# Kernel tuning notes

Measured on AMD Instinct MI355X. Metric: run time of the kernel, lower is better.

The kernel has to match this reference:

```python
import jax, jax.numpy as jnp
import numpy as np

EPS = 1e-5
HEADS, DK, DV, STRIDE, R = 8, 32, 32, 2, 4


def _conv(x, w, b, stride, pad, groups):
    y = jax.lax.conv_general_dilated(
        x, w, (stride, stride), [(pad, pad), (pad, pad)],
        dimension_numbers=('NCHW', 'OIHW', 'NCHW'),
        feature_group_count=groups)
    return y + b[None, :, None, None]


def _ln_chw(x):
    # torch F.layer_norm(x, [c, h, w]) with no affine: normalize over C,H,W per sample
    m = jnp.mean(x, axis=(1, 2, 3), keepdims=True)
    v = jnp.var(x, axis=(1, 2, 3), keepdims=True)
    return (x - m) * jax.lax.rsqrt(v + EPS)


def _bn(x, g, b, m, v):
    # eval-mode BatchNorm2d with running stats
    inv = jax.lax.rsqrt(v + EPS)
    return (x - m[None, :, None, None]) * (g * inv)[None, :, None, None] + b[None, :, None, None]


def _gelu(x):
    return jax.nn.gelu(x, approximate=False)  # torch nn.GELU default = exact erf


def _forward(x, lpu_w, lpu_b, dw_w, dw_b, wq, bq, wk, bk, wv, bv, wo, bo, pos_b,
             c1_w, c1_b, bn1_g, bn1_b, bn1_m, bn1_v,
             dw2_w, dw2_b, bn2_g, bn2_b, bn2_m, bn2_v,
             c2_w, c2_b, bn3_g, bn3_b, bn3_m, bn3_v):
    c = x.shape[1]
    # ---- LPU: depthwise 3x3 + residual ----
    x = _conv(x, lpu_w, lpu_b, 1, 1, c) + x
    b_, c, h, w = x.shape
    n = h * w
    # ---- LMHSA ----
    xn = _ln_chw(x)
    xr = xn.reshape(b_, c, n).transpose(0, 2, 1)                 # [b, N, c]
    q = (xr @ wq.T + bq).reshape(b_, n, HEADS, DK).transpose(0, 2, 1, 3)  # [b,H,N,dk]
    kv = _conv(x, dw_w, dw_b, STRIDE, 0, c)                      # note: on x (pre-LN), as in source
    nk = kv.shape[2] * kv.shape[3]
    kvr = kv.reshape(b_, c, nk).transpose(0, 2, 1)               # [b, Nk, c]
    k = (kvr @ wk.T + bk).reshape(b_, nk, HEADS, DK).transpose(0, 2, 1, 3)
    v = (kvr @ wv.T + bv).reshape(b_, nk, HEADS, DV).transpose(0, 2, 1, 3)
    att = jnp.einsum('bhid,bhjd->bhij', q, k) * (DK ** -0.5) + pos_b
    att = jax.nn.softmax(att, axis=-1)
    tmp = jnp.einsum('bhij,bhjd->bhid', att, v).transpose(0, 2, 1, 3).reshape(b_, n, HEADS * DV)
    # source does .view(b, d, h, w) on a contiguous [b, N, d] tensor -> raw row-major reinterpret
    x = (tmp @ wo.T + bo).reshape(b_, c, h, w) + x
    # ---- IRFFN ----
    t = _ln_chw(x)
    t = _gelu(_bn(_conv(t, c1_w, c1_b, 1, 0, 1), bn1_g, bn1_b, bn1_m, bn1_v))
    t = _gelu(_bn(_conv(t, dw2_w, dw2_b, 1, 1, t.shape[1]), bn2_g, bn2_b, bn2_m, bn2_v))
    t = _bn(_conv(t, c2_w, c2_b, 1, 0, 1), bn3_g, bn3_b, bn3_m, bn3_v)
    return x + t


def setup_inputs() -> dict:
    key = jax.random.key(0)
    ks = jax.random.split(key, 20)
    B_, C, H, W = 32, 256, 28, 28
    Cm = C * R
    N = H * W
    Nk = (H // STRIDE) * (W // STRIDE)
    r = lambda i, shape, s=0.02: jax.random.normal(ks[i], shape, jnp.float32) * s
    z = lambda n_: jnp.zeros((n_,), jnp.float32)
    o = lambda n_: jnp.ones((n_,), jnp.float32)
    return dict(
        x=jax.random.normal(ks[0], (B_, C, H, W), jnp.float32),
        lpu_w=r(1, (C, 1, 3, 3), 0.1), lpu_b=z(C),
        dw_w=r(2, (C, 1, STRIDE, STRIDE), 0.1), dw_b=z(C),
        wq=r(3, (HEADS * DK, C)), bq=z(HEADS * DK),
        wk=r(4, (HEADS * DK, C)), bk=z(HEADS * DK),
        wv=r(5, (HEADS * DV, C)), bv=z(HEADS * DV),
        wo=r(6, (C, HEADS * DK)), bo=z(C),
        pos_b=jax.random.normal(ks[7], (1, HEADS, N, Nk), jnp.float32),
        c1_w=r(8, (Cm, C, 1, 1)), c1_b=z(Cm),
        bn1_g=o(Cm), bn1_b=z(Cm), bn1_m=r(9, (Cm,), 0.1),
        bn1_v=jax.random.uniform(ks[10], (Cm,), jnp.float32, 0.5, 1.5),
        dw2_w=r(11, (Cm, 1, 3, 3), 0.1), dw2_b=z(Cm),
        bn2_g=o(Cm), bn2_b=z(Cm), bn2_m=r(12, (Cm,), 0.1),
        bn2_v=jax.random.uniform(ks[13], (Cm,), jnp.float32, 0.5, 1.5),
        c2_w=r(14, (C, Cm, 1, 1)), c2_b=z(C),
        bn3_g=o(C), bn3_b=z(C), bn3_m=r(15, (C,), 0.1),
        bn3_v=jax.random.uniform(ks[16], (C,), jnp.float32, 0.5, 1.5),
    )


def reference(x, lpu_w, lpu_b, dw_w, dw_b, wq, bq, wk, bk, wv, bv, wo, bo, pos_b,
              c1_w, c1_b, bn1_g, bn1_b, bn1_m, bn1_v,
              dw2_w, dw2_b, bn2_g, bn2_b, bn2_m, bn2_v,
              c2_w, c2_b, bn3_g, bn3_b, bn3_m, bn3_v):
    return _forward(x, lpu_w, lpu_b, dw_w, dw_b, wq, bq, wk, bk, wv, bv, wo, bo, pos_b,
                    c1_w, c1_b, bn1_g, bn1_b, bn1_m, bn1_v,
                    dw2_w, dw2_b, bn2_g, bn2_b, bn2_m, bn2_v,
                    c2_w, c2_b, bn3_g, bn3_b, bn3_m, bn3_v)
```

## Files before the change

### kernel.cpp

```cpp
#include <hip/hip_runtime.h>
#include <math.h>

#define B_ 32
#define C_ 256
#define H_ 28
#define W_ 28
#define NPIX 784
#define HK 14
#define NKPIX 196
#define CM 1024
#define EPS_ 1e-5f
#define LN_INVN (1.0f / (C_ * NPIX))

typedef __attribute__((ext_vector_type(8))) short short8;
typedef __attribute__((ext_vector_type(4))) short short4_;
typedef __attribute__((ext_vector_type(4))) float float4_;

__device__ __forceinline__ float gelu_f(float x) {
    float u = x * fmaf(x * x, 0.0713548163f, 1.5957691216f);
    return x / (1.f + __expf(-u));
}
__device__ __forceinline__ short f2bf(float f) {
    union { float f; unsigned u; } x; x.f = f;
    unsigned r = x.u + 0x7FFF + ((x.u >> 16) & 1);
    return (short)(r >> 16);
}
__device__ __forceinline__ float bf2f(short s) {
    union { unsigned u; float f; } x; x.u = ((unsigned)(unsigned short)s) << 16;
    return x.f;
}
__device__ __forceinline__ void gld16(const short* g, short* l) {
    __builtin_amdgcn_global_load_lds((const __attribute__((address_space(1))) void*)g,
                                     (__attribute__((address_space(3))) void*)l,
                                     16, 0, 0);
}

__global__ void wconv_kernel(const float* __restrict__ wq, const float* __restrict__ wk,
                             const float* __restrict__ wv, const float* __restrict__ wo,
                             const float* __restrict__ c1, const float* __restrict__ c2,
                             short* __restrict__ dst) {
    int idx = blockIdx.x * 256 + threadIdx.x;
    const float* src; int off;
    if (idx < 65536)       { src = wq; off = idx; }
    else if (idx < 131072) { src = wk; off = idx - 65536; }
    else if (idx < 196608) { src = wv; off = idx - 131072; }
    else if (idx < 262144) { src = wo; off = idx - 196608; }
    else if (idx < 524288) { src = c1; off = idx - 262144; }
    else                   { src = c2; off = idx - 524288; }
    dst[idx] = f2bf(src[off]);
}

__global__ void dwprep_kernel(const float* __restrict__ dww, const float* __restrict__ dwb,
                              const float* __restrict__ g2, const float* __restrict__ b2,
                              const float* __restrict__ m2, const float* __restrict__ v2,
                              const float* __restrict__ c1b, const float* __restrict__ g1,
                              const float* __restrict__ b1, const float* __restrict__ m1,
                              const float* __restrict__ v1,
                              const float* __restrict__ c2b, const float* __restrict__ g3,
                              const float* __restrict__ b3, const float* __restrict__ m3,
                              const float* __restrict__ v3,
                              float* __restrict__ wt, float* __restrict__ sc2,
                              float* __restrict__ sh2, float* __restrict__ sc1,
                              float* __restrict__ sh1, float* __restrict__ sc3,
                              float* __restrict__ sh3, float* __restrict__ st2) {
    int cm = blockIdx.x * 256 + threadIdx.x;
    if (blockIdx.x == 0 && threadIdx.x < 64) st2[threadIdx.x] = 0.f;
    float sc = g2[cm] * rsqrtf(v2[cm] + EPS_);
    sc2[cm] = sc;
    sh2[cm] = (dwb[cm] - m2[cm]) * sc + b2[cm];
    float s1 = g1[cm] * rsqrtf(v1[cm] + EPS_);
    sc1[cm] = s1;
    sh1[cm] = (c1b[cm] - m1[cm]) * s1 + b1[cm];
    if (cm < 256) {
        float s3 = g3[cm] * rsqrtf(v3[cm] + EPS_);
        sc3[cm] = s3;
        sh3[cm] = (c2b[cm] - m3[cm]) * s3 + b3[cm];
    }
    #pragma unroll
    for (int tap = 0; tap < 9; ++tap) wt[tap * 1024 + cm] = dww[cm * 9 + tap];
}

__global__ void lnreduce_kernel(const float* __restrict__ part, int cnt,
                                float* __restrict__ out) {
    int b = blockIdx.x;
    const float* p = part + (long)b * cnt * 2;
    float s = 0.f, s2 = 0.f;
    for (int i = threadIdx.x; i < cnt; i += 256) {
        s += p[i * 2];
        s2 += p[i * 2 + 1];
    }
    #pragma unroll
    for (int o = 32; o > 0; o >>= 1) {
        s += __shfl_down(s, o);
        s2 += __shfl_down(s2, o);
    }
    __shared__ float ss[4][2];
    int wv = threadIdx.x >> 6;
    if ((threadIdx.x & 63) == 0) { ss[wv][0] = s; ss[wv][1] = s2; }
    __syncthreads();
    if (threadIdx.x == 0) {
        out[b * 2]     = ss[0][0] + ss[1][0] + ss[2][0] + ss[3][0];
        out[b * 2 + 1] = ss[0][1] + ss[1][1] + ss[2][1] + ss[3][1];
    }
}

__global__ void lpu_kernel(const float* __restrict__ x, const float* __restrict__ w,
                           const float* __restrict__ bias, float* __restrict__ out,
                           float* __restrict__ part) {
    int idx4 = blockIdx.x * 256 + threadIdx.x;
    int chunk = idx4 % 196;
    int plane = idx4 / 196;
    int c = plane & 255;
    int p0 = chunk * 4;
    int py = p0 / W_, px0 = p0 % W_;
    const float* xp = x + (long)plane * NPIX;
    const float* wc = w + c * 9;
    float4 cc = *(const float4*)(xp + py * W_ + px0);
    float bb = bias[c];
    float acc0 = bb + cc.x, acc1 = bb + cc.y, acc2 = bb + cc.z, acc3 = bb + cc.w;
    #pragma unroll
    for (int dy = -1; dy <= 1; ++dy) {
        int yy = py + dy;
        if (yy < 0 || yy >= H_) continue;
        float4 v = (dy == 0) ? cc : *(const float4*)(xp + yy * W_ + px0);
        float vm1 = (px0 > 0)  ? xp[yy * W_ + px0 - 1] : 0.f;
        float v4  = (px0 < 24) ? xp[yy * W_ + px0 + 4] : 0.f;
        float w0 = wc[(dy + 1) * 3], w1 = wc[(dy + 1) * 3 + 1], w2 = wc[(dy + 1) * 3 + 2];
        acc0 += w0 * vm1 + w1 * v.x + w2 * v.y;
        acc1 += w0 * v.x + w1 * v.y + w2 * v.z;
        acc2 += w0 * v.y + w1 * v.z + w2 * v.w;
        acc3 += w0 * v.z + w1 * v.w + w2 * v4;
    }
    *(float4*)(out + (long)plane * NPIX + p0) = make_float4(acc0, acc1, acc2, acc3);
    float s = acc0 + acc1 + acc2 + acc3;
    float s2 = acc0 * acc0 + acc1 * acc1 + acc2 * acc2 + acc3 * acc3;
    #pragma unroll
    for (int o = 32; o > 0; o >>= 1) {
        s += __shfl_down(s, o);
        s2 += __shfl_down(s2, o);
    }
    __shared__ float ss[4][2];
    int wv = threadIdx.x >> 6;
    if ((threadIdx.x & 63) == 0) { ss[wv][0] = s; ss[wv][1] = s2; }
    __syncthreads();
    if (threadIdx.x == 0) {
        part[blockIdx.x * 2]     = ss[0][0] + ss[1][0] + ss[2][0] + ss[3][0];
        part[blockIdx.x * 2 + 1] = ss[0][1] + ss[1][1] + ss[2][1] + ss[3][1];
    }
}

__global__ void tln_kernel(const float* __restrict__ X, const float* __restrict__ st,
                           short* __restrict__ Y) {
    __shared__ float tile[32][33];
    int p0 = blockIdx.x * 32, c0 = blockIdx.y * 32, b = blockIdx.z;
    int tr = threadIdx.x >> 5, tc = threadIdx.x & 31;
    #pragma unroll
    for (int r = 0; r < 4; ++r) {
        int c = c0 + tr + r * 8, p = p0 + tc;
        tile[tr + r * 8][tc] = (p < NPIX) ? X[((long)b * C_ + c) * NPIX + p] : 0.f;
    }
    float sm = st[b * 2] * LN_INVN;
    float lr = rsqrtf(st[b * 2 + 1] * LN_INVN - sm * sm + EPS_);
    __syncthreads();
    #pragma unroll
    for (int r = 0; r < 4; ++r) {
        int p = p0 + tr + r * 8, c = c0 + tc;
        if (p < NPIX) Y[((long)b * NPIX + p) * C_ + c] = f2bf((tile[tc][tr + r * 8] - sm) * lr);
    }
}

__global__ void kvconv_kernel(const float* __restrict__ x1, const float* __restrict__ w,
                              const float* __restrict__ bias, short* __restrict__ out) {
    int idx = blockIdx.x * 256 + threadIdx.x;
    if (idx >= B_ * NKPIX * C_) return;
    int c = idx & 255;
    int rest = idx >> 8;
    int p = rest % NKPIX;
    int b = rest / NKPIX;
    int yo = p / HK, xo = p % HK;
    const float* xb = x1 + ((long)b * C_ + c) * NPIX;
    const float* wc = w + c * 4;
    float a = bias[c]
            + wc[0] * xb[(2 * yo) * W_ + 2 * xo]     + wc[1] * xb[(2 * yo) * W_ + 2 * xo + 1]
            + wc[2] * xb[(2 * yo + 1) * W_ + 2 * xo] + wc[3] * xb[(2 * yo + 1) * W_ + 2 * xo + 1];
    out[idx] = f2bf(a);
}

template <int EPI, int SWZ>
__global__ __launch_bounds__(256) void mfma_gemm(
    const short* __restrict__ Act, const short* __restrict__ Wb,
    int M, int N, int K,
    const float* __restrict__ bias,
    const float* __restrict__ g, const float* __restrict__ bb,
    const float* __restrict__ res, float* __restrict__ opart,
    short* __restrict__ outh, float* __restrict__ outf) {
    __shared__ short As[2 * 128 * 32];
    __shared__ short Bs[2 * 128 * 32];
    __shared__ float red[16][3];
    const int t = threadIdx.x;
    int ix, jy;
    if (SWZ) {
        const int nwg = gridDim.x;
        const int chunk = nwg >> 3;
        const int swz = (blockIdx.x & 7) * chunk + (blockIdx.x >> 3);
        const int ny = N >> 7;
        jy = swz & (ny - 1);
        ix = swz / ny;
    } else {
        ix = blockIdx.x; jy = blockIdx.y;
    }
    const int m0 = ix * 128;
    const int n0 = jy * 128;
    const int w = t >> 6, lane = t & 63;
    const int wm = (w & 1) * 64, wn = (w >> 1) * 64;
    const int col = lane & 15, quad = lane >> 4;

    float4_ acc[4][4];
    #pragma unroll
    for (int i = 0; i < 4; ++i)
        #pragma unroll
        for (int j = 0; j < 4; ++j)
            acc[i][j] = (float4_){0.f, 0.f, 0.f, 0.f};

    const int l4 = lane >> 2;
    const int segsw = (lane & 3) ^ ((l4 ^ (l4 >> 2)) & 3);
    const short* gA = Act + (long)(m0 + w * 16 + l4) * K + segsw * 8;
    const short* gB = Wb  + (long)(n0 + w * 16 + l4) * K + segsw * 8;
    const long rs64 = (long)64 * K;
    const int woff = w * 512;

    const int nk = K >> 5;
    {
        short* dA = As + woff;
        short* dB = Bs + woff;
        gld16(gA, dA);
        gld16(gA + rs64, dA + 2048);
        gld16(gB, dB);
        gld16(gB + rs64, dB + 2048);
    }
    const int slotsw = (quad ^ ((col & 3) ^ ((col >> 2) & 3))) * 8;

    for (int kt = 0; kt < nk; ++kt) {
        __syncthreads();
        const int cur = (kt & 1) * 4096;
        if (kt + 1 < nk) {
            const int nxtoff = ((kt + 1) & 1) * 4096 + woff;
            const int k0 = (kt + 1) * 32;
            gld16(gA + k0, As + nxtoff);
            gld16(gA + rs64 + k0, As + nxtoff + 2048);
            gld16(gB + k0, Bs + nxtoff);
            gld16(gB + rs64 + k0, Bs + nxtoff + 2048);
        }
        short8 af[4], bf[4];
        #pragma unroll
        for (int i = 0; i < 4; ++i)
            af[i] = *(const short8*)(As + cur + (wm + i * 16 + col) * 32 + slotsw);
        #pragma unroll
        for (int j = 0; j < 4; ++j)
            bf[j] = *(const short8*)(Bs + cur + (wn + j * 16 + col) * 32 + slotsw);
        #pragma unroll
        for (int i = 0; i < 4; ++i)
            #pragma unroll
            for (int j = 0; j < 4; ++j)
                acc[i][j] = __builtin_amdgcn_mfma_f32_16x16x32_bf16(af[i], bf[j], acc[i][j], 0, 0, 0);
    }

    #pragma unroll
    for (int i = 0; i < 4; ++i) {
        const int pbase = m0 + wm + i * 16 + quad * 4;
        float s1 = 0.f, s2s = 0.f;
        int bsmp = 0, psmp = 0;
        if (EPI == 3) { bsmp = pbase / NPIX; psmp = pbase - bsmp * NPIX; }
        #pragma unroll
        for (int j = 0; j < 4; ++j) {
            const int oc = n0 + wn + j * 16 + col;
            if (EPI == 0) {
                float cb = bias[oc];
                #pragma unroll
                for (int r = 0; r < 4; ++r)
                    outh[(long)(pbase + r) * N + oc] = f2bf(acc[i][j][r] + cb);
            } else if (EPI == 1) {
                float sc = g[oc];
                float sh = bb[oc];
                #pragma unroll
                for (int r = 0; r < 4; ++r)
                    outh[(long)(pbase + r) * N + oc] =
                        f2bf(gelu_f(fmaf(acc[i][j][r], sc, sh)));
            } else if (EPI == 2) {
                float cb = bias[oc];
                #pragma unroll
                for (int r = 0; r < 4; ++r) {
                    long jj = (long)(pbase + r) * 256 + oc;
                    float val = acc[i][j][r] + cb + res[jj];
                    outf[jj] = val;
                    s1 += val; s2s += val * val;
                }
            } else {
                float sc = g[oc];
                float sh = bb[oc];
                long basei = ((long)bsmp * 256 + oc) * NPIX + psmp;
                float4 rv = *(const float4*)(res + basei);
                float4 y;
                y.x = fmaf(acc[i][j][0], sc, sh) + rv.x;
                y.y = fmaf(acc[i][j][1], sc, sh) + rv.y;
                y.z = fmaf(acc[i][j][2], sc, sh) + rv.z;
                y.w = fmaf(acc[i][j][3], sc, sh) + rv.w;
                *(float4*)(outf + basei) = y;
            }
        }
        if (EPI == 2) {
            #pragma unroll
            for (int o = 32; o > 0; o >>= 1) {
                s1 += __shfl_down(s1, o);
                s2s += __shfl_down(s2s, o);
            }
            if (lane == 0) {
                red[w * 4 + i][0] = (float)(pbase / NPIX);
                red[w * 4 + i][1] = s1;
                red[w * 4 + i][2] = s2s;
            }
        }
    }
    if (EPI == 2) {
        __syncthreads();
        if (t == 0) {
            int bsA = (int)red[0][0], bsB = -1;
            float a1 = 0.f, a2 = 0.f, b1 = 0.f, b2 = 0.f;
            #pragma unroll
            for (int e = 0; e < 16; ++e) {
                int bs = (int)red[e][0];
                if (bs == bsA) { a1 += red[e][1]; a2 += red[e][2]; }
                else           { bsB = bs; b1 += red[e][1]; b2 += red[e][2]; }
            }
            atomicAdd(&opart[bsA * 2], a1);
            atomicAdd(&opart[bsA * 2 + 1], a2);
            if (bsB >= 0) {
                atomicAdd(&opart[bsB * 2], b1);
                atomicAdd(&opart[bsB * 2 + 1], b2);
            }
        }
    }
}

__global__ __launch_bounds__(256) void attn_kernel(const short* __restrict__ q,
                                                   const short* __restrict__ k,
                                                   const short* __restrict__ v,
                                                   const float* __restrict__ pos_b,
                                                   short* __restrict__ out) {
    __shared__ short Ks[208 * 40];
    __shared__ short Vt[32 * 232];
    __shared__ float Ls[128];
    const int qt0 = blockIdx.x * 128;
    const int h = blockIdx.y;
    const int b = blockIdx.z;
    const int t = threadIdx.x;
    const short8 z8 = {0, 0, 0, 0, 0, 0, 0, 0};
    for (int e = t; e < 832; e += 256) {
        int row = e >> 2, seg = e & 3;
        short8 v8 = (row < NKPIX)
            ? *(const short8*)(k + ((long)(b * NKPIX + row)) * 256 + h * 32 + seg * 8) : z8;
        *(short8*)(Ks + row * 40 + seg * 8) = v8;
    }
    for (int e = t; e < 784; e += 256) {
        int key = e >> 2, seg = e & 3;
        short8 tv = *(const short8*)(v + ((long)(b * NKPIX + key)) * 256 + h * 32 + seg * 8);
        #pragma unroll
        for (int j = 0; j < 8; ++j) Vt[(seg * 8 + j) * 232 + key] = tv[j];
    }
    for (int e = t; e < 32 * 36; e += 256) {
        Vt[(e / 36) * 232 + 196 + (e % 36)] = 0;
    }
    __syncthreads();

    const int w = t >> 6, lane = t & 63;
    const int col = lane & 15, quad = lane >> 4;
    const float scale = 0.17677669529663689f;
    const float4_ z4 = {0.f, 0.f, 0.f, 0.f};

    short8 bq_[2];
    int qrow[2]; bool qvalid[2];
    const float* prow[2];
    #pragma unroll
    for (int i = 0; i < 2; ++i) {
        qrow[i] = qt0 + w * 32 + i * 16 + col;
        qvalid[i] = qrow[i] < NPIX;
        int qe = qvalid[i] ? qrow[i] : 0;
        bq_[i] = *(const short8*)(q + ((long)(b * NPIX + qe)) * 256 + h * 32 + quad * 8);
        prow[i] = pos_b + ((long)h * NPIX + qrow[i]) * NKPIX;
    }

    float4_ accO[2][2];
    #pragma unroll
    for (int i = 0; i < 2; ++i)
        #pragma unroll
        for (int nt = 0; nt < 2; ++nt) accO[i][nt] = z4;
    float lsum[2] = {0.f, 0.f};

    const int srcA = col + 32 * (quad & 1);
    const int srcB = srcA + 16;
    const bool hihalf = quad >= 2;

    #pragma unroll
    for (int kc = 0; kc < 4; ++kc) {
        const int base = kc * 64;
        const int ntn = (kc == 3) ? 1 : 4;
        unsigned long long v64[2][4];
        if (kc == 3) { v64[0][1] = 0ULL; v64[1][1] = 0ULL; }
        #pragma unroll
        for (int nt = 0; nt < 4; ++nt) {
            if (nt >= ntn) continue;
            short8 afk = *(const short8*)(Ks + (base + nt * 16 + col) * 40 + quad * 8);
            int keybase = base + nt * 16 + quad * 4;
            bool kval = keybase < NKPIX;
            #pragma unroll
            for (int i = 0; i < 2; ++i) {
                float4_ s4 = __builtin_amdgcn_mfma_f32_16x16x32_bf16(afk, bq_[i], z4, 0, 0, 0);
                float4 pv = make_float4(0.f, 0.f, 0.f, 0.f);
                bool valid = kval && qvalid[i];
                if (valid)
                    pv = *(const float4*)(prow[i] + keybase);
                float p0 = valid ? __expf(s4[0] * scale + pv.x) : 0.f;
                float p1 = valid ? __expf(s4[1] * scale + pv.y) : 0.f;
                float p2 = valid ? __expf(s4[2] * scale + pv.z) : 0.f;
                float p3 = valid ? __expf(s4[3] * scale + pv.w) : 0.f;
                lsum[i] += p0 + p1 + p2 + p3;
                unsigned lo = ((unsigned)(unsigned short)f2bf(p1) << 16) |
                              (unsigned)(unsigned short)f2bf(p0);
                unsigned hi = ((unsigned)(unsigned short)f2bf(p3) << 16) |
                              (unsigned)(unsigned short)f2bf(p2);
                v64[i][nt] = ((unsigned long long)hi << 32) | lo;
            }
        }
        const int ksn = (kc == 3) ? 1 : 2;
        #pragma unroll
        for (int ks = 0; ks < 2; ++ks) {
            if (ks >= ksn) continue;
            #pragma unroll
            for (int i = 0; i < 2; ++i) {
                unsigned long long sel = hihalf ? v64[i][2 * ks + 1] : v64[i][2 * ks];
                unsigned long long flo = __shfl(sel, srcA, 64);
                unsigned long long fhi = __shfl(sel, srcB, 64);
                union { unsigned long long u; short s[4]; } ul, uh;
                ul.u = flo; uh.u = fhi;
                short8 afp = { ul.s[0], ul.s[1], ul.s[2], ul.s[3],
                               uh.s[0], uh.s[1], uh.s[2], uh.s[3] };
                #pragma unroll
                for (int nt = 0; nt < 2; ++nt) {
                    short8 bfv = *(const short8*)(Vt + (nt * 16 + col) * 232 + base + ks * 32 + quad * 8);
                    accO[i][nt] = __builtin_amdgcn_mfma_f32_16x16x32_bf16(afp, bfv, accO[i][nt], 0, 0, 0);
                }
            }
        }
    }
    #pragma unroll
    for (int i = 0; i < 2; ++i) {
        float s = lsum[i];
        s += __shfl_xor(s, 16);
        s += __shfl_xor(s, 32);
        if (quad == 0) Ls[w * 32 + i * 16 + col] = 1.f / s;
    }
    __builtin_amdgcn_s_waitcnt(0);
    #pragma unroll
    for (int i = 0; i < 2; ++i) {
        int qb0 = qt0 + w * 32 + i * 16 + quad * 4;
        #pragma unroll
        for (int r = 0; r < 4; ++r) {
            int qq = qb0 + r;
            if (qq >= NPIX) continue;
            float rinv = Ls[w * 32 + i * 16 + quad * 4 + r];
            #pragma unroll
            for (int nt = 0; nt < 2; ++nt)
                out[((long)(b * NPIX + qq)) * 256 + h * 32 + nt * 16 + col] =
                    f2bf(accO[i][nt][r] * rinv);
        }
    }
}

__global__ __launch_bounds__(256) void dwgelu_kernel(
    const short* __restrict__ t2, const float* __restrict__ wt,
    const float* __restrict__ sc2, const float* __restrict__ sh2,
    short* __restrict__ t3) {
    const int nchunk = 3136 / 8;
    int bid = blockIdx.x;
    int swz = (bid & 7) * nchunk + (bid >> 3);
    int idx = swz * 256 + threadIdx.x;
    int cm8 = idx & 127;
    int rest = idx >> 7;
    int grp = rest % 196;
    int b = rest / 196;
    int py0 = (grp / 28) * 4;
    int px = grp % 28;
    int cm0 = cm8 * 8;
    const short* tb = t2 + ((long)b * NPIX) * CM + cm0;

    float wv[9][8];
    #pragma unroll
    for (int tp = 0; tp < 9; ++tp) {
        float4 a = *(const float4*)(wt + tp * 1024 + cm0);
        float4 bq = *(const float4*)(wt + tp * 1024 + cm0 + 4);
        wv[tp][0] = a.x;  wv[tp][1] = a.y;  wv[tp][2] = a.z;  wv[tp][3] = a.w;
        wv[tp][4] = bq.x; wv[tp][5] = bq.y; wv[tp][6] = bq.z; wv[tp][7] = bq.w;
    }

    float acc[4][8];
    #pragma unroll
    for (int k = 0; k < 4; ++k)
        #pragma unroll
        for (int c = 0; c < 8; ++c) acc[k][c] = 0.f;

    #pragma unroll
    for (int ro = -1; ro <= 4; ++ro) {
        int rr = py0 + ro;
        if (rr < 0 || rr >= H_) continue;
        const short* rowb = tb + (long)(rr * W_ + px) * CM;
        float fm[8], fc[8], fp[8];
        if (px > 0) {
            short8 s = *(const short8*)(rowb - CM);
            #pragma unroll
            for (int c = 0; c < 8; ++c) fm[c] = bf2f(s[c]);
        } else {
            #pragma unroll
            for (int c = 0; c < 8; ++c) fm[c] = 0.f;
        }
        {
            short8 s = *(const short8*)(rowb);
            #pragma unroll
            for (int c = 0; c < 8; ++c) fc[c] = bf2f(s[c]);
        }
        if (px < 27) {
            short8 s = *(const short8*)(rowb + CM);
            #pragma unroll
            for (int c = 0; c < 8; ++c) fp[c] = bf2f(s[c]);
        } else {
            #pragma unroll
            for (int c = 0; c < 8; ++c) fp[c] = 0.f;
        }
        #pragma unroll
        for (int k = 0; k < 4; ++k) {
            const int tr = ro - k + 1;
            if (tr < 0 || tr > 2) continue;
            #pragma unroll
            for (int c = 0; c < 8; ++c)
                acc[k][c] = fmaf(wv[tr * 3][c], fm[c],
                            fmaf(wv[tr * 3 + 1][c], fc[c],
                            fmaf(wv[tr * 3 + 2][c], fp[c], acc[k][c])));
        }
    }

    float4 sa = *(const float4*)(sc2 + cm0);
    float4 sb = *(const float4*)(sc2 + cm0 + 4);
    float4 ha = *(const float4*)(sh2 + cm0);
    float4 hb = *(const float4*)(sh2 + cm0 + 4);
    float scl[8] = {sa.x, sa.y, sa.z, sa.w, sb.x, sb.y, sb.z, sb.w};
    float shf[8] = {ha.x, ha.y, ha.z, ha.w, hb.x, hb.y, hb.z, hb.w};
    #pragma unroll
    for (int k = 0; k < 4; ++k) {
        short8 ov;
        #pragma unroll
        for (int c = 0; c < 8; ++c)
            ov[c] = f2bf(gelu_f(fmaf(acc[k][c], scl[c], shf[c])));
        *(short8*)(t3 + ((long)b * NPIX + (py0 + k) * W_ + px) * CM + cm0) = ov;
    }
}

extern "C" void kernel_launch(void* const* d_in, const int* in_sizes, int n_in,
                              void* d_out, int out_size, void* d_ws, size_t ws_size,
                              hipStream_t stream) {
    const float* x     = (const float*)d_in[0];
    const float* lpu_w = (const float*)d_in[1];
    const float* lpu_b = (const float*)d_in[2];
    const float* dw_w  = (const float*)d_in[3];
    const float* dw_b  = (const float*)d_in[4];
    const float* wq    = (const float*)d_in[5];
    const float* bq    = (const float*)d_in[6];
    const float* wk    = (const float*)d_in[7];
    const float* bk    = (const float*)d_in[8];
    const float* wv    = (const float*)d_in[9];
    const float* bv    = (const float*)d_in[10];
    const float* wo    = (const float*)d_in[11];
    const float* bo    = (const float*)d_in[12];
    const float* posb  = (const float*)d_in[13];
    const float* c1_w  = (const float*)d_in[14];
    const float* c1_b  = (const float*)d_in[15];
    const float* bn1_g = (const float*)d_in[16];
    const float* bn1_b = (const float*)d_in[17];
    const float* bn1_m = (const float*)d_in[18];
    const float* bn1_v = (const float*)d_in[19];
    const float* dw2_w = (const float*)d_in[20];
    const float* dw2_b = (const float*)d_in[21];
    const float* bn2_g = (const float*)d_in[22];
    const float* bn2_b = (const float*)d_in[23];
    const float* bn2_m = (const float*)d_in[24];
    const float* bn2_v = (const float*)d_in[25];
    const float* c2_w  = (const float*)d_in[26];
    const float* c2_b  = (const float*)d_in[27];
    const float* bn3_g = (const float*)d_in[28];
    const float* bn3_b = (const float*)d_in[29];
    const float* bn3_m = (const float*)d_in[30];
    const float* bn3_v = (const float*)d_in[31];

    const long n1  = (long)B_ * C_ * NPIX;
    const long nkv = (long)B_ * C_ * NKPIX;
    const long nm  = (long)B_ * CM * NPIX;
    const int  nblk1 = (int)(n1 / 1024);
    const int  MQ = B_ * NPIX;
    const int  MKV = B_ * NKPIX;

    char* base = (char*)d_ws;
    float* x1   = (float*)base; base += n1 * 4;
    float* x2c  = (float*)base; base += n1 * 4;
    short* x1n  = (short*)base; base += n1 * 2;
    short* qb   = (short*)base; base += n1 * 2;
    short* tmpb = (short*)base; base += n1 * 2;
    short* t1n  = (short*)base; base += n1 * 2;
    short* kvb  = (short*)base; base += nkv * 2;
    short* kb   = (short*)base; base += nkv * 2;
    short* vb   = (short*)base; base += nkv * 2;
    short* t2   = (short*)base; base += nm * 2;
    short* t3   = (short*)base; base += nm * 2;
    short* wbf  = (short*)base; base += 786432L * 2;
    float* stats = (float*)base; base += 128 * 4;
    float* dwt   = (float*)base; base += 9216 * 4;
    float* dsc   = (float*)base; base += 1024 * 4;
    float* dsh   = (float*)base; base += 1024 * 4;
    float* dsc1  = (float*)base; base += 1024 * 4;
    float* dsh1  = (float*)base; base += 1024 * 4;
    float* dsc3  = (float*)base; base += 256 * 4;
    float* dsh3  = (float*)base; base += 256 * 4;
    float* part1 = (float*)base; base += (long)nblk1 * 2 * 4;
    float* outp = (float*)d_out;

    wconv_kernel<<<3072, 256, 0, stream>>>(wq, wk, wv, wo, c1_w, c2_w, wbf);
    dwprep_kernel<<<4, 256, 0, stream>>>(dw2_w, dw2_b, bn2_g, bn2_b, bn2_m, bn2_v,
                                         c1_b, bn1_g, bn1_b, bn1_m, bn1_v,
                                         c2_b, bn3_g, bn3_b, bn3_m, bn3_v,
                                         dwt, dsc, dsh, dsc1, dsh1, dsc3, dsh3,
                                         stats + 64);
    lpu_kernel<<<nblk1, 256, 0, stream>>>(x, lpu_w, lpu_b, x1, part1);
    lnreduce_kernel<<<B_, 256, 0, stream>>>(part1, nblk1 / B_, stats);
    kvconv_kernel<<<(int)((nkv + 255) / 256), 256, 0, stream>>>(x1, dw_w, dw_b, kvb);
    tln_kernel<<<dim3(25, 8, B_), 256, 0, stream>>>(x1, stats, x1n);
    mfma_gemm<0, 1><<<392, 256, 0, stream>>>(
        x1n, wbf, MQ, 256, 256, bq, nullptr, nullptr,
        nullptr, nullptr, qb, nullptr);
    mfma_gemm<0, 0><<<dim3(MKV / 128, 2), 256, 0, stream>>>(
        kvb, wbf + 65536, MKV, 256, 256, bk, nullptr, nullptr,
        nullptr, nullptr, kb, nullptr);
    mfma_gemm<0, 0><<<dim3(MKV / 128, 2), 256, 0, stream>>>(
        kvb, wbf + 131072, MKV, 256, 256, bv, nullptr, nullptr,
        nullptr, nullptr, vb, nullptr);
    attn_kernel<<<dim3(7, 8, B_), 256, 0, stream>>>(qb, kb, vb, posb, tmpb);
    mfma_gemm<2, 1><<<392, 256, 0, stream>>>(
        tmpb, wbf + 196608, MQ, 256, 256, bo, nullptr, nullptr,
        x1, stats + 64, nullptr, x2c);
    tln_kernel<<<dim3(25, 8, B_), 256, 0, stream>>>(x2c, stats + 64, t1n);
    mfma_gemm<1, 1><<<1568, 256, 0, stream>>>(
        t1n, wbf + 262144, MQ, CM, 256, nullptr, dsc1, dsh1,
        nullptr, nullptr, t2, nullptr);
    dwgelu_kernel<<<3136, 256, 0, stream>>>(t2, dwt, dsc, dsh, t3);
    mfma_gemm<3, 1><<<392, 256, 0, stream>>>(
        t3, wbf + 524288, MQ, 256, 1024, nullptr, dsc3, dsh3,
        x2c, nullptr, nullptr, outp);
}
```

Baseline: 402.1 us.

## Split attention query tile across eight waves with one 16-row tile each

The attention kernel now launches 512 threads per block, and each of the 8 waves handles a single 16-query tile instead of two. This halves per-thread register state and doubles the number of waves available to hide latency. The row normalizer is now broadcast with a wave shuffle instead of an LDS array. In exchange, each K/V tile staged in LDS is shared by more waves, and larger blocks may reduce how many blocks fit per CU.

```diff
diff --git a/kernel.cpp b/kernel.cpp
--- a/kernel.cpp
+++ b/kernel.cpp
@@ -342,32 +342,31 @@
     }
 }
 
-__global__ __launch_bounds__(256) void attn_kernel(const short* __restrict__ q,
+__global__ __launch_bounds__(512) void attn_kernel(const short* __restrict__ q,
                                                    const short* __restrict__ k,
                                                    const short* __restrict__ v,
                                                    const float* __restrict__ pos_b,
                                                    short* __restrict__ out) {
     __shared__ short Ks[208 * 40];
     __shared__ short Vt[32 * 232];
-    __shared__ float Ls[128];
     const int qt0 = blockIdx.x * 128;
     const int h = blockIdx.y;
     const int b = blockIdx.z;
     const int t = threadIdx.x;
     const short8 z8 = {0, 0, 0, 0, 0, 0, 0, 0};
-    for (int e = t; e < 832; e += 256) {
+    for (int e = t; e < 832; e += 512) {
         int row = e >> 2, seg = e & 3;
         short8 v8 = (row < NKPIX)
             ? *(const short8*)(k + ((long)(b * NKPIX + row)) * 256 + h * 32 + seg * 8) : z8;
         *(short8*)(Ks + row * 40 + seg * 8) = v8;
     }
-    for (int e = t; e < 784; e += 256) {
+    for (int e = t; e < 784; e += 512) {
         int key = e >> 2, seg = e & 3;
         short8 tv = *(const short8*)(v + ((long)(b * NKPIX + key)) * 256 + h * 32 + seg * 8);
         #pragma unroll
         for (int j = 0; j < 8; ++j) Vt[(seg * 8 + j) * 232 + key] = tv[j];
     }
-    for (int e = t; e < 32 * 36; e += 256) {
+    for (int e = t; e < 32 * 36; e += 512) {
         Vt[(e / 36) * 232 + 196 + (e % 36)] = 0;
     }
     __syncthreads();
@@ -377,24 +376,14 @@
     const float scale = 0.17677669529663689f;
     const float4_ z4 = {0.f, 0.f, 0.f, 0.f};
 
-    short8 bq_[2];
-    int qrow[2]; bool qvalid[2];
-    const float* prow[2];
-    #pragma unroll
-    for (int i = 0; i < 2; ++i) {
-        qrow[i] = qt0 + w * 32 + i * 16 + col;
-        qvalid[i] = qrow[i] < NPIX;
-        int qe = qvalid[i] ? qrow[i] : 0;
-        bq_[i] = *(const short8*)(q + ((long)(b * NPIX + qe)) * 256 + h * 32 + quad * 8);
-        prow[i] = pos_b + ((long)h * NPIX + qrow[i]) * NKPIX;
-    }
-
-    float4_ accO[2][2];
-    #pragma unroll
-    for (int i = 0; i < 2; ++i)
-        #pragma unroll
-        for (int nt = 0; nt < 2; ++nt) accO[i][nt] = z4;
-    float lsum[2] = {0.f, 0.f};
+    const int qrow = qt0 + w * 16 + col;
+    const bool qvalid = qrow < NPIX;
+    const int qe = qvalid ? qrow : 0;
+    const short8 bq_ = *(const short8*)(q + ((long)(b * NPIX + qe)) * 256 + h * 32 + quad * 8);
+    const float* prow = pos_b + ((long)h * NPIX + qrow) * NKPIX;
+
+    float4_ accO[2] = {z4, z4};
+    float lsum = 0.f;
 
     const int srcA = col + 32 * (quad & 1);
     const int srcB = srcA + 16;
@@ -404,75 +393,60 @@
     for (int kc = 0; kc < 4; ++kc) {
         const int base = kc * 64;
         const int ntn = (kc == 3) ? 1 : 4;
-        unsigned long long v64[2][4];
-        if (kc == 3) { v64[0][1] = 0ULL; v64[1][1] = 0ULL; }
+        unsigned long long v64[4];
+        if (kc == 3) v64[1] = 0ULL;
         #pragma unroll
         for (int nt = 0; nt < 4; ++nt) {
             if (nt >= ntn) continue;
             short8 afk = *(const short8*)(Ks + (base + nt * 16 + col) * 40 + quad * 8);
             int keybase = base + nt * 16 + quad * 4;
-            bool kval = keybase < NKPIX;
-            #pragma unroll
-            for (int i = 0; i < 2; ++i) {
-                float4_ s4 = __builtin_amdgcn_mfma_f32_16x16x32_bf16(afk, bq_[i], z4, 0, 0, 0);
-                float4 pv = make_float4(0.f, 0.f, 0.f, 0.f);
-                bool valid = kval && qvalid[i];
-                if (valid)
-                    pv = *(const float4*)(prow[i] + keybase);
-                float p0 = valid ? __expf(s4[0] * scale + pv.x) : 0.f;
-                float p1 = valid ? __expf(s4[1] * scale + pv.y) : 0.f;
-                float p2 = valid ? __expf(s4[2] * scale + pv.z) : 0.f;
-                float p3 = valid ? __expf(s4[3] * scale + pv.w) : 0.f;
-                lsum[i] += p0 + p1 + p2 + p3;
-                unsigned lo = ((unsigned)(unsigned short)f2bf(p1) << 16) |
-                              (unsigned)(unsigned short)f2bf(p0);
-                unsigned hi = ((unsigned)(unsigned short)f2bf(p3) << 16) |
-                              (unsigned)(unsigned short)f2bf(p2);
-                v64[i][nt] = ((unsigned long long)hi << 32) | lo;
-            }
+            bool valid = (keybase < NKPIX) && qvalid;
+            float4_ s4 = __builtin_amdgcn_mfma_f32_16x16x32_bf16(afk, bq_, z4, 0, 0, 0);
+            float4 pv = make_float4(0.f, 0.f, 0.f, 0.f);
+            if (valid)
+                pv = *(const float4*)(prow + keybase);
+            float p0 = valid ? __expf(s4[0] * scale + pv.x) : 0.f;
+            float p1 = valid ? __expf(s4[1] * scale + pv.y) : 0.f;
+            float p2 = valid ? __expf(s4[2] * scale + pv.z) : 0.f;
+            float p3 = valid ? __expf(s4[3] * scale + pv.w) : 0.f;
+            lsum += p0 + p1 + p2 + p3;
+            unsigned lo = ((unsigned)(unsigned short)f2bf(p1) << 16) |
+                          (unsigned)(unsigned short)f2bf(p0);
+            unsigned hi = ((unsigned)(unsigned short)f2bf(p3) << 16) |
+                          (unsigned)(unsigned short)f2bf(p2);
+            v64[nt] = ((unsigned long long)hi << 32) | lo;
         }
         const int ksn = (kc == 3) ? 1 : 2;
         #pragma unroll
         for (int ks = 0; ks < 2; ++ks) {
             if (ks >= ksn) continue;
-            #pragma unroll
-            for (int i = 0; i < 2; ++i) {
-                unsigned long long sel = hihalf ? v64[i][2 * ks + 1] : v64[i][2 * ks];
-                unsigned long long flo = __shfl(sel, srcA, 64);
-                unsigned long long fhi = __shfl(sel, srcB, 64);
-                union { unsigned long long u; short s[4]; } ul, uh;
-                ul.u = flo; uh.u = fhi;
-                short8 afp = { ul.s[0], ul.s[1], ul.s[2], ul.s[3],
-                               uh.s[0], uh.s[1], uh.s[2], uh.s[3] };
-                #pragma unroll
-                for (int nt = 0; nt < 2; ++nt) {
-                    short8 bfv = *(const short8*)(Vt + (nt * 16 + col) * 232 + base + ks * 32 + quad * 8);
-                    accO[i][nt] = __builtin_amdgcn_mfma_f32_16x16x32_bf16(afp, bfv, accO[i][nt], 0, 0, 0);
-                }
+            unsigned long long sel = hihalf ? v64[2 * ks + 1] : v64[2 * ks];
+            unsigned long long flo = __shfl(sel, srcA, 64);
+            unsigned long long fhi = __shfl(sel, srcB, 64);
+            union { unsigned long long u; short s[4]; } ul, uh;
+            ul.u = flo; uh.u = fhi;
+            short8 afp = { ul.s[0], ul.s[1], ul.s[2], ul.s[3],
+                           uh.s[0], uh.s[1], uh.s[2], uh.s[3] };
+            #pragma unroll
+            for (int nt = 0; nt < 2; ++nt) {
+                short8 bfv = *(const short8*)(Vt + (nt * 16 + col) * 232 + base + ks * 32 + quad * 8);
+                accO[nt] = __builtin_amdgcn_mfma_f32_16x16x32_bf16(afp, bfv, accO[nt], 0, 0, 0);
             }
         }
     }
-    #pragma unroll
-    for (int i = 0; i < 2; ++i) {
-        float s = lsum[i];
-        s += __shfl_xor(s, 16);
-        s += __shfl_xor(s, 32);
-        if (quad == 0) Ls[w * 32 + i * 16 + col] = 1.f / s;
-    }
-    __builtin_amdgcn_s_waitcnt(0);
-    #pragma unroll
-    for (int i = 0; i < 2; ++i) {
-        int qb0 = qt0 + w * 32 + i * 16 + quad * 4;
-        #pragma unroll
-        for (int r = 0; r < 4; ++r) {
-            int qq = qb0 + r;
-            if (qq >= NPIX) continue;
-            float rinv = Ls[w * 32 + i * 16 + quad * 4 + r];
-            #pragma unroll
-            for (int nt = 0; nt < 2; ++nt)
-                out[((long)(b * NPIX + qq)) * 256 + h * 32 + nt * 16 + col] =
-                    f2bf(accO[i][nt][r] * rinv);
-        }
+    float s = lsum;
+    s += __shfl_xor(s, 16);
+    s += __shfl_xor(s, 32);
+    float rinv_col = 1.f / s;
+    #pragma unroll
+    for (int r = 0; r < 4; ++r) {
+        int qq = qt0 + w * 16 + quad * 4 + r;
+        if (qq >= NPIX) continue;
+        float rinv = __shfl(rinv_col, quad * 4 + r, 64);
+        #pragma unroll
+        for (int nt = 0; nt < 2; ++nt)
+            out[((long)(b * NPIX + qq)) * 256 + h * 32 + nt * 16 + col] =
+                f2bf(accO[nt][r] * rinv);
     }
 }
 
@@ -649,7 +623,7 @@
     mfma_gemm<0, 0><<<dim3(MKV / 128, 2), 256, 0, stream>>>(
         kvb, wbf + 131072, MKV, 256, 256, bv, nullptr, nullptr,
         nullptr, nullptr, vb, nullptr);
-    attn_kernel<<<dim3(7, 8, B_), 256, 0, stream>>>(qb, kb, vb, posb, tmpb);
+    attn_kernel<<<dim3(7, 8, B_), 512, 0, stream>>>(qb, kb, vb, posb, tmpb);
     mfma_gemm<2, 1><<<392, 256, 0, stream>>>(
         tmpb, wbf + 196608, MQ, 256, 256, bo, nullptr, nullptr,
         x1, stats + 64, nullptr, x2c);
```

After: 408.0 us. About the same (+1.5%).
